# Performance work log

Measured on AMD Instinct MI355X. Metric: run time of the kernel, lower is better.

Reference implementation:

```python
import jax, jax.numpy as jnp
import numpy as np

B, L, C = 16, 3136, 96
H_, W_ = 56, 56
R = 3            # graph relations (short/medium/long range)
CTX = 2          # context relations: depthwise convs with kernels 3 and 5 (use_all_context)
RT = R + CTX
E = 131072
FFN_H = 4 * C


def setup_inputs() -> dict:
    key = jax.random.key(0)
    ks = jax.random.split(key, 16)
    s = lambda i, shape: jax.random.normal(ks[i], shape, dtype=jnp.float32) * 0.02
    return {
        "x": jax.random.normal(ks[0], (B, L, C), dtype=jnp.float32),
        "edge_index": jax.random.randint(ks[1], (2, E), 0, L),
        "edge_type": jax.random.randint(ks[2], (E,), 0, R),
        "H": H_, "W": W_,
        "norm1_g": jnp.ones((C,), jnp.float32), "norm1_b": jnp.zeros((C,), jnp.float32),
        "value_w": s(3, (C, C)), "value_b": jnp.zeros((C,), jnp.float32),
        "gate_w": s(4, (C, RT)), "gate_b": jnp.zeros((RT,), jnp.float32),
        "ctx_k3": s(5, (C, 1, 3, 3)), "ctx_b3": jnp.zeros((C,), jnp.float32),
        "ctx_k5": s(6, (C, 1, 5, 5)), "ctx_b5": jnp.zeros((C,), jnp.float32),
        "rel_w": s(7, (RT * C, C)), "rel_b": jnp.zeros((C,), jnp.float32),
        "proj_w": s(8, (C, C)), "proj_b": jnp.zeros((C,), jnp.float32),
        "norm2_g": jnp.ones((C,), jnp.float32), "norm2_b": jnp.zeros((C,), jnp.float32),
        "fc1_w": s(9, (C, FFN_H)), "fc1_b": jnp.zeros((FFN_H,), jnp.float32),
        "fc2_w": s(10, (FFN_H, C)), "fc2_b": jnp.zeros((C,), jnp.float32),
    }


def layer_norm(x, g, b, eps=1e-5):
    mu = x.mean(-1, keepdims=True)
    var = ((x - mu) ** 2).mean(-1, keepdims=True)
    return (x - mu) * jax.lax.rsqrt(var + eps) * g + b


def dwconv(x_bchw, k, b):
    out = jax.lax.conv_general_dilated(
        x_bchw, k, window_strides=(1, 1), padding="SAME",
        feature_group_count=x_bchw.shape[1],
        dimension_numbers=("NCHW", "OIHW", "NCHW"))
    return out + b[None, :, None, None]


def grmp(x, edge_index, edge_type, H, W,
         value_w, value_b, gate_w, gate_b,
         ctx_k3, ctx_b3, ctx_k5, ctx_b5, rel_w, rel_b):
    # Gated relational message passing over RT relations.
    Bx, Lx, Cx = x.shape
    v = x @ value_w + value_b                               # [B,L,C] node values
    src, dst = edge_index[0], edge_index[1]
    seg = dst * R + edge_type                               # fused (node, relation) segment id
    cnt = jax.ops.segment_sum(jnp.ones((E,), x.dtype), seg, num_segments=Lx * R)
    cnt = jnp.maximum(cnt, 1.0)[None, :, None]
    # mean-aggregate messages per (dst node, relation)
    agg = jax.vmap(lambda vb: jax.ops.segment_sum(vb[src], seg, num_segments=Lx * R))(v)
    agg = (agg / cnt).reshape(Bx, Lx, R, Cx)                # [B,L,R,C]
    # context relations: depthwise convs on the spatial layout of values
    v_img = v.reshape(Bx, H, W, Cx).transpose(0, 3, 1, 2)   # [B,C,H,W]
    c3 = dwconv(v_img, ctx_k3, ctx_b3).transpose(0, 2, 3, 1).reshape(Bx, Lx, 1, Cx)
    c5 = dwconv(v_img, ctx_k5, ctx_b5).transpose(0, 2, 3, 1).reshape(Bx, Lx, 1, Cx)
    upd = jnp.concatenate([agg, c3, c5], axis=2)            # [B,L,RT,C]
    gate = jax.nn.sigmoid(x @ gate_w + gate_b)              # [B,L,RT] per-relation gates
    upd = upd * gate[..., None]
    out = upd.reshape(Bx, Lx, RT * Cx) @ rel_w + rel_b      # relation mixing
    return jax.nn.gelu(out, approximate=False)


def reference(x, edge_index, edge_type, H, W,
              norm1_g, norm1_b, value_w, value_b, gate_w, gate_b,
              ctx_k3, ctx_b3, ctx_k5, ctx_b5, rel_w, rel_b,
              proj_w, proj_b, norm2_g, norm2_b, fc1_w, fc1_b, fc2_w, fc2_b):
    h = layer_norm(x, norm1_g, norm1_b)
    h = grmp(h, edge_index, edge_type, H, W, value_w, value_b, gate_w, gate_b,
             ctx_k3, ctx_b3, ctx_k5, ctx_b5, rel_w, rel_b)
    h = h @ proj_w + proj_b
    x = x + h                                               # residual 1 (drop_path = identity)
    h2 = layer_norm(x, norm2_g, norm2_b)
    h2 = jax.nn.gelu(h2 @ fc1_w + fc1_b, approximate=False) @ fc2_w + fc2_b
    return x + h2                                           # residual 2
```

## Files before the change

### kernel.cpp

```cpp
#include <hip/hip_runtime.h>
#include <hip/hip_bf16.h>
#include <math.h>

#define BB 16
#define LL 3136
#define CC 96
#define HH 56
#define WW 56
#define RR 3
#define RTOT 5
#define EE 131072
#define NR (BB*LL)
#define NSEG (LL*RR)
#define FFN 384

typedef __attribute__((ext_vector_type(8))) short bf16x8;
typedef __attribute__((ext_vector_type(4))) float f32x4;
typedef __attribute__((ext_vector_type(8))) unsigned short u16x8;

__device__ __forceinline__ unsigned short f2bf(float f) {
    unsigned u = __builtin_bit_cast(unsigned, f);
    unsigned r = u + 0x7FFF + ((u >> 16) & 1);
    return (unsigned short)(r >> 16);
}
__device__ __forceinline__ float bf2f(unsigned short h) {
    unsigned u = ((unsigned)h) << 16;
    return __builtin_bit_cast(float, u);
}

__device__ __forceinline__ float gelu_exact(float v) {
    return 0.5f * v * (1.0f + erff(v * 0.70710678118654752440f));
}

__global__ __launch_bounds__(256) void ln_kernel(const float* __restrict__ x,
                                                 const float* __restrict__ g,
                                                 const float* __restrict__ bta,
                                                 float* __restrict__ out, int nrows)
{
    int wave = threadIdx.x >> 6;
    int lane = threadIdx.x & 63;
    int row  = blockIdx.x * 4 + wave;
    if (row >= nrows) return;
    const float* xr = x + (size_t)row * CC;
    float v0 = xr[lane];
    float v1 = (lane < 32) ? xr[64 + lane] : 0.f;
    float s = v0 + v1;
    #pragma unroll
    for (int off = 32; off; off >>= 1) s += __shfl_xor(s, off);
    float mean = s * (1.f / 96.f);
    float d0 = v0 - mean;
    float d1 = (lane < 32) ? (v1 - mean) : 0.f;
    float q = d0 * d0 + d1 * d1;
    #pragma unroll
    for (int off = 32; off; off >>= 1) q += __shfl_xor(q, off);
    float rstd = rsqrtf(q * (1.f / 96.f) + 1e-5f);
    out[(size_t)row * CC + lane] = d0 * rstd * g[lane] + bta[lane];
    if (lane < 32)
        out[(size_t)row * CC + 64 + lane] = d1 * rstd * g[64 + lane] + bta[64 + lane];
}

#define SPL_TOT 138240
__global__ __launch_bounds__(256) void prep_split(const float* __restrict__ vw,
                                                  const float* __restrict__ rw,
                                                  const float* __restrict__ pw,
                                                  const float* __restrict__ f1w,
                                                  const float* __restrict__ f2w,
                                                  unsigned short* __restrict__ bhi,
                                                  unsigned short* __restrict__ blo)
{
    int t = blockIdx.x * 256 + threadIdx.x;
    if (t >= SPL_TOT) return;
    const float* src; int K, N, local;
    if (t < 9216)        { src = vw;  K = 96;  N = 96;  local = t; }
    else if (t < 55296)  { src = rw;  K = 480; N = 96;  local = t - 9216; }
    else if (t < 64512)  { src = pw;  K = 96;  N = 96;  local = t - 55296; }
    else if (t < 101376) { src = f1w; K = 96;  N = 384; local = t - 64512; }
    else                 { src = f2w; K = 384; N = 96;  local = t - 101376; }
    int n = local / K, k = local - n * K;
    float f = src[(size_t)k * N + n];
    unsigned short h = f2bf(f);
    unsigned short l = f2bf(f - bf2f(h));
    bhi[t] = h;
    blo[t] = l;
}

__global__ __launch_bounds__(256) void prep_convw(const float* __restrict__ k3,
                                                  const float* __restrict__ k5,
                                                  float* __restrict__ k3t,
                                                  float* __restrict__ k5t)
{
    int t = blockIdx.x * 256 + threadIdx.x;
    if (t < 864) {
        int c = t / 9, tap = t - c * 9;
        k3t[tap * 96 + c] = k3[t];
    } else if (t < 864 + 2400) {
        int u = t - 864;
        int c = u / 25, tap = u - c * 25;
        k5t[tap * 96 + c] = k5[u];
    }
}

template<int ACT, bool RES, bool PERM, bool ABF16, bool OUTBF16>
__global__ __launch_bounds__(256) void gemm_mfma(const void* __restrict__ Ain,
                                                 const unsigned short* __restrict__ Bhi,
                                                 const unsigned short* __restrict__ Blo,
                                                 const float* __restrict__ bias,
                                                 const float* __restrict__ res,
                                                 void* __restrict__ outv,
                                                 int M, int N, int K)
{
    __shared__ unsigned short AsH[64 * 32];
    __shared__ unsigned short AsL[ABF16 ? 8 : 64 * 32];
    __shared__ unsigned short BsH[96 * 32], BsL[96 * 32];
    const int tid  = threadIdx.x;
    const int bm   = blockIdx.x * 64;
    const int bn   = blockIdx.y * 96;
    const int lane = tid & 63;
    const int w    = tid >> 6;
    const int wm   = w >> 1, wn = w & 1;
    const int r16  = lane & 15, q = lane >> 4;

    f32x4 acc[2][3];
    #pragma unroll
    for (int mt = 0; mt < 2; mt++)
        #pragma unroll
        for (int nt = 0; nt < 3; nt++) acc[mt][nt] = (f32x4)0.f;

    const int arow = tid >> 2;
    const int akq  = (tid & 3) * 8;
    const int bn_  = tid >> 1;
    const int bh_  = (tid & 1) * 16;

    for (int kc = 0; kc < K; kc += 32) {
        __syncthreads();
        if constexpr (ABF16) {
            const unsigned short* Ab = (const unsigned short*)Ain;
            u16x8 h8 = *(const u16x8*)&Ab[(size_t)(bm + arow) * K + kc + akq];
            *(u16x8*)&AsH[arow * 32 + akq] = h8;
        } else {
            const float* A = (const float*)Ain;
            const float* ap = A + (size_t)(bm + arow) * K + kc + akq;
            float4 f0 = *(const float4*)ap;
            float4 f1 = *(const float4*)(ap + 4);
            float ff[8] = {f0.x, f0.y, f0.z, f0.w, f1.x, f1.y, f1.z, f1.w};
            u16x8 h8, l8;
            #pragma unroll
            for (int j = 0; j < 8; j++) {
                unsigned short h = f2bf(ff[j]);
                h8[j] = h;
                l8[j] = f2bf(ff[j] - bf2f(h));
            }
            *(u16x8*)&AsH[arow * 32 + akq] = h8;
            *(u16x8*)&AsL[arow * 32 + akq] = l8;
        }
        if (tid < 192) {
            const unsigned short* bph = Bhi + (size_t)(bn + bn_) * K + kc + bh_;
            const unsigned short* bpl = Blo + (size_t)(bn + bn_) * K + kc + bh_;
            u16x8 h0 = *(const u16x8*)bph;
            u16x8 h1 = *(const u16x8*)(bph + 8);
            u16x8 l0 = *(const u16x8*)bpl;
            u16x8 l1 = *(const u16x8*)(bpl + 8);
            *(u16x8*)&BsH[bn_ * 32 + bh_ + 0] = h0;
            *(u16x8*)&BsH[bn_ * 32 + bh_ + 8] = h1;
            *(u16x8*)&BsL[bn_ * 32 + bh_ + 0] = l0;
            *(u16x8*)&BsL[bn_ * 32 + bh_ + 8] = l1;
        }
        __syncthreads();
        bf16x8 aH[2], aL[2], bH[3], bL[3];
        #pragma unroll
        for (int mt = 0; mt < 2; mt++) {
            int rbase = (wm * 32 + mt * 16 + r16) * 32 + q * 8;
            aH[mt] = *(const bf16x8*)&AsH[rbase];
            if constexpr (!ABF16) aL[mt] = *(const bf16x8*)&AsL[rbase];
        }
        #pragma unroll
        for (int nt = 0; nt < 3; nt++) {
            int cbase = (wn * 48 + nt * 16 + r16) * 32 + q * 8;
            bH[nt] = *(const bf16x8*)&BsH[cbase];
            bL[nt] = *(const bf16x8*)&BsL[cbase];
        }
        #pragma unroll
        for (int mt = 0; mt < 2; mt++)
            #pragma unroll
            for (int nt = 0; nt < 3; nt++) {
                acc[mt][nt] = __builtin_amdgcn_mfma_f32_16x16x32_bf16(aH[mt], bH[nt], acc[mt][nt], 0, 0, 0);
                acc[mt][nt] = __builtin_amdgcn_mfma_f32_16x16x32_bf16(aH[mt], bL[nt], acc[mt][nt], 0, 0, 0);
                if constexpr (!ABF16)
                    acc[mt][nt] = __builtin_amdgcn_mfma_f32_16x16x32_bf16(aL[mt], bH[nt], acc[mt][nt], 0, 0, 0);
            }
    }

    #pragma unroll
    for (int mt = 0; mt < 2; mt++) {
        #pragma unroll
        for (int nt = 0; nt < 3; nt++) {
            int col = bn + wn * 48 + nt * 16 + r16;
            float bv = bias[col];
            #pragma unroll
            for (int r = 0; r < 4; r++) {
                int row = bm + wm * 32 + mt * 16 + q * 4 + r;
                float val = acc[mt][nt][r] + bv;
                if (ACT == 1) val = gelu_exact(val);
                if (RES) val += res[(size_t)row * N + col];
                size_t orow;
                if (PERM) {
                    int b = row / LL;
                    int l = row - b * LL;
                    orow = (size_t)l * BB + b;
                } else {
                    orow = (size_t)row;
                }
                if constexpr (OUTBF16)
                    ((unsigned short*)outv)[orow * N + col] = f2bf(val);
                else
                    ((float*)outv)[orow * N + col] = val;
            }
        }
    }
}

__global__ __launch_bounds__(256) void gate_kernel(const float* __restrict__ h,
                                                   const float* __restrict__ gw,
                                                   const float* __restrict__ gb,
                                                   float* __restrict__ gate)
{
    int wave = threadIdx.x >> 6;
    int lane = threadIdx.x & 63;
    int row  = blockIdx.x * 4 + wave;
    if (row >= NR) return;
    const float* hr = h + (size_t)row * CC;
    float v0 = hr[lane];
    float v1 = (lane < 32) ? hr[64 + lane] : 0.f;
    #pragma unroll
    for (int r = 0; r < RTOT; r++) {
        float s = v0 * gw[lane * RTOT + r];
        if (lane < 32) s += v1 * gw[(64 + lane) * RTOT + r];
        #pragma unroll
        for (int off = 32; off; off >>= 1) s += __shfl_xor(s, off);
        if (lane == r) gate[(size_t)row * RTOT + r] = 1.f / (1.f + expf(-(s + gb[r])));
    }
}

__global__ void hist_kernel(const int* __restrict__ ei, const int* __restrict__ et,
                            int* __restrict__ cnt)
{
    int e = blockIdx.x * 256 + threadIdx.x;
    if (e >= EE) return;
    int dst = ei[EE + e];
    int r   = et[e];
    atomicAdd(&cnt[dst * RR + r], 1);
}

__global__ __launch_bounds__(1024) void scan_kernel(const int* __restrict__ cnt,
                                                    int* __restrict__ colptr,
                                                    float* __restrict__ invcnt)
{
    __shared__ int wsum[16];
    int tid = threadIdx.x, wid = tid >> 6, lane = tid & 63;
    int carry = 0;
    for (int base = 0; base < NSEG; base += 1024) {
        int idx = base + tid;
        int v = (idx < NSEG) ? cnt[idx] : 0;
        if (idx < NSEG) invcnt[idx] = 1.f / (float)max(v, 1);
        int sc = v;
        #pragma unroll
        for (int off = 1; off < 64; off <<= 1) {
            int o = __shfl_up(sc, off);
            if (lane >= off) sc += o;
        }
        if (lane == 63) wsum[wid] = sc;
        __syncthreads();
        if (wid == 0) {
            int w = (lane < 16) ? wsum[lane] : 0;
            #pragma unroll
            for (int off = 1; off < 16; off <<= 1) {
                int o = __shfl_up(w, off);
                if (lane >= off) w += o;
            }
            if (lane < 16) wsum[lane] = w;
        }
        __syncthreads();
        int woff = (wid > 0) ? wsum[wid - 1] : 0;
        if (idx < NSEG) colptr[idx] = carry + woff + sc - v;
        carry += wsum[15];
        __syncthreads();
    }
    if (tid == 0) colptr[NSEG] = carry;
}

__global__ void scatter_kernel(const int* __restrict__ ei, const int* __restrict__ et,
                               const int* __restrict__ colptr, int* __restrict__ fill,
                               int* __restrict__ esorted)
{
    int e = blockIdx.x * 256 + threadIdx.x;
    if (e >= EE) return;
    int src = ei[e];
    int dst = ei[EE + e];
    int seg = dst * RR + et[e];
    int pos = colptr[seg] + atomicAdd(&fill[seg], 1);
    esorted[pos] = src;
}

__device__ __forceinline__ void unp6(const unsigned short* p, float* f) {
    unsigned u0 = *(const unsigned*)(p + 0);
    unsigned u1 = *(const unsigned*)(p + 2);
    unsigned u2 = *(const unsigned*)(p + 4);
    f[0] = bf2f((unsigned short)u0); f[1] = bf2f((unsigned short)(u0 >> 16));
    f[2] = bf2f((unsigned short)u1); f[3] = bf2f((unsigned short)(u1 >> 16));
    f[4] = bf2f((unsigned short)u2); f[5] = bf2f((unsigned short)(u2 >> 16));
}
__device__ __forceinline__ void pack6(unsigned short* p, const float* f) {
    unsigned u0 = (unsigned)f2bf(f[0]) | ((unsigned)f2bf(f[1]) << 16);
    unsigned u1 = (unsigned)f2bf(f[2]) | ((unsigned)f2bf(f[3]) << 16);
    unsigned u2 = (unsigned)f2bf(f[4]) | ((unsigned)f2bf(f[5]) << 16);
    *(unsigned*)(p + 0) = u0;
    *(unsigned*)(p + 2) = u1;
    *(unsigned*)(p + 4) = u2;
}

__global__ __launch_bounds__(256) void aggconv_kernel(
        const unsigned short* __restrict__ vp,
        const float* __restrict__ gate,
        const int* __restrict__ colptr, const int* __restrict__ esorted,
        const float* __restrict__ invcnt,
        const float* __restrict__ k3t, const float* __restrict__ b3,
        const float* __restrict__ k5t, const float* __restrict__ b5,
        unsigned short* __restrict__ updg)
{
    int l = blockIdx.x;
    int t = threadIdx.x;
    int b = t >> 4;
    int g = t & 15;
    int ch = g * 6;

    float gs[RTOT];
    #pragma unroll
    for (int r = 0; r < RTOT; r++) gs[r] = gate[((size_t)b * LL + l) * RTOT + r];
    size_t ob = ((size_t)b * LL + l) * (RTOT * CC);

    #pragma unroll
    for (int r = 0; r < RR; r++) {
        int s0 = colptr[l * RR + r], s1 = colptr[l * RR + r + 1];
        float acc[6] = {0.f, 0.f, 0.f, 0.f, 0.f, 0.f};
        int src = (s0 < s1) ? esorted[s0] : 0;
        for (int e = s0; e < s1; e++) {
            int nsrc = (e + 1 < s1) ? esorted[e + 1] : 0;
            float f[6];
            unp6(vp + ((size_t)src * BB + b) * CC + ch, f);
            #pragma unroll
            for (int j = 0; j < 6; j++) acc[j] += f[j];
            src = nsrc;
        }
        float sc = invcnt[l * RR + r] * gs[r];
        float o[6];
        #pragma unroll
        for (int j = 0; j < 6; j++) o[j] = acc[j] * sc;
        unsigned short ov[6];
        pack6(ov, o);
        *(unsigned*)(updg + ob + r * CC + ch + 0) = *(unsigned*)(ov + 0);
        *(unsigned*)(updg + ob + r * CC + ch + 2) = *(unsigned*)(ov + 2);
        *(unsigned*)(updg + ob + r * CC + ch + 4) = *(unsigned*)(ov + 4);
    }

    int h0 = l / WW, w0 = l - (l / WW) * WW;
    float a3[6], a5[6];
    #pragma unroll
    for (int j = 0; j < 6; j++) { a3[j] = b3[ch + j]; a5[j] = b5[ch + j]; }
    #pragma unroll
    for (int kh = -2; kh <= 2; kh++) {
        int hh = h0 + kh; if (hh < 0 || hh >= HH) continue;
        #pragma unroll
        for (int kw = -2; kw <= 2; kw++) {
            int ww = w0 + kw; if (ww < 0 || ww >= WW) continue;
            float f[6];
            unp6(vp + ((size_t)(hh * WW + ww) * BB + b) * CC + ch, f);
            int tap5 = (kh + 2) * 5 + (kw + 2);
            #pragma unroll
            for (int j = 0; j < 6; j++) a5[j] += f[j] * k5t[tap5 * CC + ch + j];
            if (kh >= -1 && kh <= 1 && kw >= -1 && kw <= 1) {
                int tap3 = (kh + 1) * 3 + (kw + 1);
                #pragma unroll
                for (int j = 0; j < 6; j++) a3[j] += f[j] * k3t[tap3 * CC + ch + j];
            }
        }
    }
    float o3[6], o5[6];
    #pragma unroll
    for (int j = 0; j < 6; j++) { o3[j] = a3[j] * gs[3]; o5[j] = a5[j] * gs[4]; }
    unsigned short v3[6], v5[6];
    pack6(v3, o3);
    pack6(v5, o5);
    *(unsigned*)(updg + ob + 3 * CC + ch + 0) = *(unsigned*)(v3 + 0);
    *(unsigned*)(updg + ob + 3 * CC + ch + 2) = *(unsigned*)(v3 + 2);
    *(unsigned*)(updg + ob + 3 * CC + ch + 4) = *(unsigned*)(v3 + 4);
    *(unsigned*)(updg + ob + 4 * CC + ch + 0) = *(unsigned*)(v5 + 0);
    *(unsigned*)(updg + ob + 4 * CC + ch + 2) = *(unsigned*)(v5 + 2);
    *(unsigned*)(updg + ob + 4 * CC + ch + 4) = *(unsigned*)(v5 + 4);
}

extern "C" void kernel_launch(void* const* d_in, const int* in_sizes, int n_in,
                              void* d_out, int out_size, void* d_ws, size_t ws_size,
                              hipStream_t stream)
{
    const float* x       = (const float*)d_in[0];
    const int*   ei      = (const int*)d_in[1];
    const int*   et      = (const int*)d_in[2];
    const float* n1g     = (const float*)d_in[5];
    const float* n1b     = (const float*)d_in[6];
    const float* value_w = (const float*)d_in[7];
    const float* value_b = (const float*)d_in[8];
    const float* gate_w  = (const float*)d_in[9];
    const float* gate_b  = (const float*)d_in[10];
    const float* k3      = (const float*)d_in[11];
    const float* b3      = (const float*)d_in[12];
    const float* k5      = (const float*)d_in[13];
    const float* b5      = (const float*)d_in[14];
    const float* rel_w   = (const float*)d_in[15];
    const float* rel_b   = (const float*)d_in[16];
    const float* proj_w  = (const float*)d_in[17];
    const float* proj_b  = (const float*)d_in[18];
    const float* n2g     = (const float*)d_in[19];
    const float* n2b     = (const float*)d_in[20];
    const float* fc1_w   = (const float*)d_in[21];
    const float* fc1_b   = (const float*)d_in[22];
    const float* fc2_w   = (const float*)d_in[23];
    const float* fc2_b   = (const float*)d_in[24];
    float* out = (float*)d_out;

    float* w = (float*)d_ws;
    const size_t SZ_ROW = (size_t)NR * CC;
    float* hbuf   = w;
    float* vbuf   = hbuf + SZ_ROW;
    float* gateb  = vbuf + SZ_ROW;
    float* updg   = gateb + (size_t)NR * RTOT;
    int*   ibase  = (int*)(updg + (size_t)NR * RTOT * CC);
    int*   cnt     = ibase;
    int*   colptr  = cnt + NSEG;
    int*   fill    = colptr + NSEG + 1;
    int*   esorted = fill + NSEG;
    float* invcnt  = (float*)(esorted + EE);
    unsigned short* bhi = (unsigned short*)(invcnt + NSEG);
    unsigned short* blo = bhi + SPL_TOT;
    float* k3t = (float*)(blo + SPL_TOT);
    float* k5t = k3t + 864;

    unsigned short* vp_bf   = (unsigned short*)vbuf;
    unsigned short* g1_bf   = (unsigned short*)hbuf;
    unsigned short* updg_bf = (unsigned short*)updg;
    unsigned short* hid_bf  = (unsigned short*)updg;
    float* x1 = vbuf;

    hipMemsetAsync(cnt, 0, NSEG * sizeof(int), stream);
    hipMemsetAsync(fill, 0, NSEG * sizeof(int), stream);

    prep_split<<<(SPL_TOT + 255) / 256, 256, 0, stream>>>(value_w, rel_w, proj_w, fc1_w, fc2_w, bhi, blo);
    prep_convw<<<(864 + 2400 + 255) / 256, 256, 0, stream>>>(k3, k5, k3t, k5t);
    ln_kernel<<<NR / 4, 256, 0, stream>>>(x, n1g, n1b, hbuf, NR);
    gemm_mfma<0, false, true, false, true><<<dim3(NR / 64, 1), 256, 0, stream>>>(hbuf, bhi + 0, blo + 0, value_b, nullptr, vp_bf, NR, 96, 96);
    gate_kernel<<<NR / 4, 256, 0, stream>>>(hbuf, gate_w, gate_b, gateb);
    hist_kernel<<<EE / 256, 256, 0, stream>>>(ei, et, cnt);
    scan_kernel<<<1, 1024, 0, stream>>>(cnt, colptr, invcnt);
    scatter_kernel<<<EE / 256, 256, 0, stream>>>(ei, et, colptr, fill, esorted);
    aggconv_kernel<<<dim3(LL), 256, 0, stream>>>(vp_bf, gateb, colptr, esorted, invcnt,
                                                 k3t, b3, k5t, b5, updg_bf);
    gemm_mfma<1, false, false, true, true><<<dim3(NR / 64, 1), 256, 0, stream>>>(updg_bf, bhi + 9216, blo + 9216, rel_b, nullptr, g1_bf, NR, 96, 480);
    gemm_mfma<0, true, false, true, false><<<dim3(NR / 64, 1), 256, 0, stream>>>(g1_bf, bhi + 55296, blo + 55296, proj_b, x, x1, NR, 96, 96);
    ln_kernel<<<NR / 4, 256, 0, stream>>>(x1, n2g, n2b, hbuf, NR);
    gemm_mfma<1, false, false, false, true><<<dim3(NR / 64, 4), 256, 0, stream>>>(hbuf, bhi + 64512, blo + 64512, fc1_b, nullptr, hid_bf, NR, 384, 96);
    gemm_mfma<0, true, false, true, false><<<dim3(NR / 64, 1), 256, 0, stream>>>(hid_bf, bhi + 101376, blo + 101376, fc2_b, x1, out, NR, 96, 384);
}
```

Measured before the change: 379.1 us.

## Fuse gate into layernorm, widen aggconv to 8-channel vectors, remap block order

The gate projection and sigmoid are now computed inside the first layernorm kernel, which removes a separate kernel launch and a re-read of the normalized activations. The aggregation/conv kernel now has each thread handle 8 bf16 channels with 16-byte vector loads and stores, using 192 threads per block instead of 256 with 6 channels each. Its block-to-node mapping is also interleaved, which changes the order in which spatial neighbours are visited and may affect cache locality. The wider vectors raise per-thread register use.

```diff
diff --git a/kernel.cpp b/kernel.cpp
--- a/kernel.cpp
+++ b/kernel.cpp
@@ -32,10 +32,15 @@
     return 0.5f * v * (1.0f + erff(v * 0.70710678118654752440f));
 }
 
+template<bool GATE>
 __global__ __launch_bounds__(256) void ln_kernel(const float* __restrict__ x,
                                                  const float* __restrict__ g,
                                                  const float* __restrict__ bta,
-                                                 float* __restrict__ out, int nrows)
+                                                 float* __restrict__ out,
+                                                 const float* __restrict__ gw,
+                                                 const float* __restrict__ gb,
+                                                 float* __restrict__ gate,
+                                                 int nrows)
 {
     int wave = threadIdx.x >> 6;
     int lane = threadIdx.x & 63;
@@ -54,9 +59,21 @@
     #pragma unroll
     for (int off = 32; off; off >>= 1) q += __shfl_xor(q, off);
     float rstd = rsqrtf(q * (1.f / 96.f) + 1e-5f);
-    out[(size_t)row * CC + lane] = d0 * rstd * g[lane] + bta[lane];
-    if (lane < 32)
-        out[(size_t)row * CC + 64 + lane] = d1 * rstd * g[64 + lane] + bta[64 + lane];
+    float o0 = d0 * rstd * g[lane] + bta[lane];
+    float o1 = 0.f;
+    if (lane < 32) o1 = d1 * rstd * g[64 + lane] + bta[64 + lane];
+    out[(size_t)row * CC + lane] = o0;
+    if (lane < 32) out[(size_t)row * CC + 64 + lane] = o1;
+    if constexpr (GATE) {
+        #pragma unroll
+        for (int r = 0; r < RTOT; r++) {
+            float sg = o0 * gw[lane * RTOT + r];
+            if (lane < 32) sg += o1 * gw[(64 + lane) * RTOT + r];
+            #pragma unroll
+            for (int off = 32; off; off >>= 1) sg += __shfl_xor(sg, off);
+            if (lane == r) gate[(size_t)row * RTOT + r] = 1.f / (1.f + expf(-(sg + gb[r])));
+        }
+    }
 }
 
 #define SPL_TOT 138240
@@ -219,28 +236,6 @@
     }
 }
 
-__global__ __launch_bounds__(256) void gate_kernel(const float* __restrict__ h,
-                                                   const float* __restrict__ gw,
-                                                   const float* __restrict__ gb,
-                                                   float* __restrict__ gate)
-{
-    int wave = threadIdx.x >> 6;
-    int lane = threadIdx.x & 63;
-    int row  = blockIdx.x * 4 + wave;
-    if (row >= NR) return;
-    const float* hr = h + (size_t)row * CC;
-    float v0 = hr[lane];
-    float v1 = (lane < 32) ? hr[64 + lane] : 0.f;
-    #pragma unroll
-    for (int r = 0; r < RTOT; r++) {
-        float s = v0 * gw[lane * RTOT + r];
-        if (lane < 32) s += v1 * gw[(64 + lane) * RTOT + r];
-        #pragma unroll
-        for (int off = 32; off; off >>= 1) s += __shfl_xor(s, off);
-        if (lane == r) gate[(size_t)row * RTOT + r] = 1.f / (1.f + expf(-(s + gb[r])));
-    }
-}
-
 __global__ void hist_kernel(const int* __restrict__ ei, const int* __restrict__ et,
                             int* __restrict__ cnt)
 {
@@ -301,24 +296,19 @@
     esorted[pos] = src;
 }
 
-__device__ __forceinline__ void unp6(const unsigned short* p, float* f) {
-    unsigned u0 = *(const unsigned*)(p + 0);
-    unsigned u1 = *(const unsigned*)(p + 2);
-    unsigned u2 = *(const unsigned*)(p + 4);
-    f[0] = bf2f((unsigned short)u0); f[1] = bf2f((unsigned short)(u0 >> 16));
-    f[2] = bf2f((unsigned short)u1); f[3] = bf2f((unsigned short)(u1 >> 16));
-    f[4] = bf2f((unsigned short)u2); f[5] = bf2f((unsigned short)(u2 >> 16));
-}
-__device__ __forceinline__ void pack6(unsigned short* p, const float* f) {
-    unsigned u0 = (unsigned)f2bf(f[0]) | ((unsigned)f2bf(f[1]) << 16);
-    unsigned u1 = (unsigned)f2bf(f[2]) | ((unsigned)f2bf(f[3]) << 16);
-    unsigned u2 = (unsigned)f2bf(f[4]) | ((unsigned)f2bf(f[5]) << 16);
-    *(unsigned*)(p + 0) = u0;
-    *(unsigned*)(p + 2) = u1;
-    *(unsigned*)(p + 4) = u2;
-}
-
-__global__ __launch_bounds__(256) void aggconv_kernel(
+__device__ __forceinline__ void unp8(const unsigned short* p, float* f) {
+    u16x8 v = *(const u16x8*)p;
+    #pragma unroll
+    for (int j = 0; j < 8; j++) f[j] = bf2f(v[j]);
+}
+__device__ __forceinline__ void pack8(unsigned short* p, const float* f) {
+    u16x8 v;
+    #pragma unroll
+    for (int j = 0; j < 8; j++) v[j] = f2bf(f[j]);
+    *(u16x8*)p = v;
+}
+
+__global__ __launch_bounds__(192) void aggconv_kernel(
         const unsigned short* __restrict__ vp,
         const float* __restrict__ gate,
         const int* __restrict__ colptr, const int* __restrict__ esorted,
@@ -327,11 +317,12 @@
         const float* __restrict__ k5t, const float* __restrict__ b5,
         unsigned short* __restrict__ updg)
 {
-    int l = blockIdx.x;
+    int bid = blockIdx.x;
+    int l = (bid & 7) * (LL / 8) + (bid >> 3);
     int t = threadIdx.x;
-    int b = t >> 4;
-    int g = t & 15;
-    int ch = g * 6;
+    int b = t / 12;
+    int g = t - b * 12;
+    int ch = g * 8;
 
     float gs[RTOT];
     #pragma unroll
@@ -341,61 +332,52 @@
     #pragma unroll
     for (int r = 0; r < RR; r++) {
         int s0 = colptr[l * RR + r], s1 = colptr[l * RR + r + 1];
-        float acc[6] = {0.f, 0.f, 0.f, 0.f, 0.f, 0.f};
+        float acc[8] = {0.f, 0.f, 0.f, 0.f, 0.f, 0.f, 0.f, 0.f};
         int src = (s0 < s1) ? esorted[s0] : 0;
         for (int e = s0; e < s1; e++) {
             int nsrc = (e + 1 < s1) ? esorted[e + 1] : 0;
-            float f[6];
-            unp6(vp + ((size_t)src * BB + b) * CC + ch, f);
-            #pragma unroll
-            for (int j = 0; j < 6; j++) acc[j] += f[j];
+            float f[8];
+            unp8(vp + ((size_t)src * BB + b) * CC + ch, f);
+            #pragma unroll
+            for (int j = 0; j < 8; j++) acc[j] += f[j];
             src = nsrc;
         }
         float sc = invcnt[l * RR + r] * gs[r];
-        float o[6];
-        #pragma unroll
-        for (int j = 0; j < 6; j++) o[j] = acc[j] * sc;
-        unsigned short ov[6];
-        pack6(ov, o);
-        *(unsigned*)(updg + ob + r * CC + ch + 0) = *(unsigned*)(ov + 0);
-        *(unsigned*)(updg + ob + r * CC + ch + 2) = *(unsigned*)(ov + 2);
-        *(unsigned*)(updg + ob + r * CC + ch + 4) = *(unsigned*)(ov + 4);
+        float o[8];
+        #pragma unroll
+        for (int j = 0; j < 8; j++) o[j] = acc[j] * sc;
+        pack8(updg + ob + r * CC + ch, o);
     }
 
     int h0 = l / WW, w0 = l - (l / WW) * WW;
-    float a3[6], a5[6];
-    #pragma unroll
-    for (int j = 0; j < 6; j++) { a3[j] = b3[ch + j]; a5[j] = b5[ch + j]; }
+    float a3[8], a5[8];
+    #pragma unroll
+    for (int j = 0; j < 8; j++) { a3[j] = b3[ch + j]; a5[j] = b5[ch + j]; }
     #pragma unroll
     for (int kh = -2; kh <= 2; kh++) {
         int hh = h0 + kh; if (hh < 0 || hh >= HH) continue;
         #pragma unroll
         for (int kw = -2; kw <= 2; kw++) {
             int ww = w0 + kw; if (ww < 0 || ww >= WW) continue;
-            float f[6];
-            unp6(vp + ((size_t)(hh * WW + ww) * BB + b) * CC + ch, f);
+            float f[8];
+            unp8(vp + ((size_t)(hh * WW + ww) * BB + b) * CC + ch, f);
             int tap5 = (kh + 2) * 5 + (kw + 2);
-            #pragma unroll
-            for (int j = 0; j < 6; j++) a5[j] += f[j] * k5t[tap5 * CC + ch + j];
+            const float* w5p = &k5t[tap5 * CC + ch];
+            #pragma unroll
+            for (int j = 0; j < 8; j++) a5[j] += f[j] * w5p[j];
             if (kh >= -1 && kh <= 1 && kw >= -1 && kw <= 1) {
                 int tap3 = (kh + 1) * 3 + (kw + 1);
+                const float* w3p = &k3t[tap3 * CC + ch];
                 #pragma unroll
-                for (int j = 0; j < 6; j++) a3[j] += f[j] * k3t[tap3 * CC + ch + j];
+                for (int j = 0; j < 8; j++) a3[j] += f[j] * w3p[j];
             }
         }
     }
-    float o3[6], o5[6];
-    #pragma unroll
-    for (int j = 0; j < 6; j++) { o3[j] = a3[j] * gs[3]; o5[j] = a5[j] * gs[4]; }
-    unsigned short v3[6], v5[6];
-    pack6(v3, o3);
-    pack6(v5, o5);
-    *(unsigned*)(updg + ob + 3 * CC + ch + 0) = *(unsigned*)(v3 + 0);
-    *(unsigned*)(updg + ob + 3 * CC + ch + 2) = *(unsigned*)(v3 + 2);
-    *(unsigned*)(updg + ob + 3 * CC + ch + 4) = *(unsigned*)(v3 + 4);
-    *(unsigned*)(updg + ob + 4 * CC + ch + 0) = *(unsigned*)(v5 + 0);
-    *(unsigned*)(updg + ob + 4 * CC + ch + 2) = *(unsigned*)(v5 + 2);
-    *(unsigned*)(updg + ob + 4 * CC + ch + 4) = *(unsigned*)(v5 + 4);
+    float o3[8], o5[8];
+    #pragma unroll
+    for (int j = 0; j < 8; j++) { o3[j] = a3[j] * gs[3]; o5[j] = a5[j] * gs[4]; }
+    pack8(updg + ob + 3 * CC + ch, o3);
+    pack8(updg + ob + 4 * CC + ch, o5);
 }
 
 extern "C" void kernel_launch(void* const* d_in, const int* in_sizes, int n_in,
@@ -455,17 +437,16 @@
 
     prep_split<<<(SPL_TOT + 255) / 256, 256, 0, stream>>>(value_w, rel_w, proj_w, fc1_w, fc2_w, bhi, blo);
     prep_convw<<<(864 + 2400 + 255) / 256, 256, 0, stream>>>(k3, k5, k3t, k5t);
-    ln_kernel<<<NR / 4, 256, 0, stream>>>(x, n1g, n1b, hbuf, NR);
+    ln_kernel<true><<<NR / 4, 256, 0, stream>>>(x, n1g, n1b, hbuf, gate_w, gate_b, gateb, NR);
     gemm_mfma<0, false, true, false, true><<<dim3(NR / 64, 1), 256, 0, stream>>>(hbuf, bhi + 0, blo + 0, value_b, nullptr, vp_bf, NR, 96, 96);
-    gate_kernel<<<NR / 4, 256, 0, stream>>>(hbuf, gate_w, gate_b, gateb);
     hist_kernel<<<EE / 256, 256, 0, stream>>>(ei, et, cnt);
     scan_kernel<<<1, 1024, 0, stream>>>(cnt, colptr, invcnt);
     scatter_kernel<<<EE / 256, 256, 0, stream>>>(ei, et, colptr, fill, esorted);
-    aggconv_kernel<<<dim3(LL), 256, 0, stream>>>(vp_bf, gateb, colptr, esorted, invcnt,
+    aggconv_kernel<<<dim3(LL), 192, 0, stream>>>(vp_bf, gateb, colptr, esorted, invcnt,
                                                  k3t, b3, k5t, b5, updg_bf);
     gemm_mfma<1, false, false, true, true><<<dim3(NR / 64, 1), 256, 0, stream>>>(updg_bf, bhi + 9216, blo + 9216, rel_b, nullptr, g1_bf, NR, 96, 480);
     gemm_mfma<0, true, false, true, false><<<dim3(NR / 64, 1), 256, 0, stream>>>(g1_bf, bhi + 55296, blo + 55296, proj_b, x, x1, NR, 96, 96);
-    ln_kernel<<<NR / 4, 256, 0, stream>>>(x1, n2g, n2b, hbuf, NR);
+    ln_kernel<false><<<NR / 4, 256, 0, stream>>>(x1, n2g, n2b, hbuf, nullptr, nullptr, nullptr, NR);
     gemm_mfma<1, false, false, false, true><<<dim3(NR / 64, 4), 256, 0, stream>>>(hbuf, bhi + 64512, blo + 64512, fc1_b, nullptr, hid_bf, NR, 384, 96);
     gemm_mfma<0, true, false, true, false><<<dim3(NR / 64, 1), 256, 0, stream>>>(hid_bf, bhi + 101376, blo + 101376, fc2_b, x1, out, NR, 96, 384);
 }
```

Result: faster. 364.9 us (-3.8%).
